# Kernel tuning notes

Measured on AMD Instinct MI355X. Metric: run time of the kernel, lower is better.

Reference implementation:

```python
import jax, jax.numpy as jnp
import numpy as np

N, E, CIN, COUT = 50000, 800000, 61, 64
EPS = 1e-5


def batchnorm(h, g, b):
    # BatchNorm1d in training mode: batch stats (biased variance), affine
    m = jnp.mean(h, axis=0)
    v = jnp.var(h, axis=0)
    return g * (h - m) * jax.lax.rsqrt(v + EPS) + b


def setup_inputs() -> dict:
    key = jax.random.key(0)
    ks = jax.random.split(key, 7)
    x = jax.random.normal(ks[0], (N, CIN), jnp.float32)
    pos = jax.random.normal(ks[1], (N, 3), jnp.float32)
    edge_index = jax.random.randint(ks[2], (2, E), 0, N, dtype=jnp.int64)
    s1 = 1.0 / np.sqrt(CIN + 3)
    s2 = 1.0 / np.sqrt(COUT)
    ss = 1.0 / np.sqrt(CIN)
    W1 = jax.random.normal(ks[3], (CIN + 3, COUT), jnp.float32) * s1
    b1 = jnp.zeros((COUT,), jnp.float32)
    W2 = jax.random.normal(ks[4], (COUT, COUT), jnp.float32) * s2
    b2 = jnp.zeros((COUT,), jnp.float32)
    Ws = jax.random.normal(ks[5], (CIN, COUT), jnp.float32) * ss
    bs = jnp.zeros((COUT,), jnp.float32)
    ones = jnp.ones((COUT,), jnp.float32)
    zeros = jnp.zeros((COUT,), jnp.float32)
    return {
        "x": x, "pos": pos, "edge_index": edge_index,
        "W1": W1, "b1": b1, "g1": ones, "be1": zeros,
        "W2": W2, "b2": b2, "g2": ones, "be2": zeros,
        "Ws": Ws, "bs": bs, "gs": ones, "bes": zeros,
        "gf": ones, "bef": zeros,
    }


def reference(x, pos, edge_index, W1, b1, g1, be1, W2, b2, g2, be2,
              Ws, bs, gs, bes, gf, bef):
    src, dst = edge_index[0], edge_index[1]  # j -> i (source_to_target)
    # per-edge message: [x_j, pos_j - pos_i]  -> [E, CIN+3]
    msg = jnp.concatenate([x[src], pos[src] - pos[dst]], axis=-1)
    # local_nn = MLP([CIN+3, COUT, COUT]) with per-layer Lin -> ReLU -> BN
    h = batchnorm(jax.nn.relu(msg @ W1 + b1), g1, be1)
    h = batchnorm(jax.nn.relu(h @ W2 + b2), g2, be2)
    # scatter-max aggregation to destination nodes
    agg = jax.ops.segment_max(h, dst, num_segments=N)
    agg = jnp.where(jnp.isneginf(agg), 0.0, agg)  # nodes with no incoming edges
    # residual shortcut (Linear + BN since CIN != COUT)
    identity = batchnorm(x @ Ws + bs, gs, bes)
    return jax.nn.relu(batchnorm(agg, gf, bef) + identity)
```

## Files before the change

kernel.cpp:

```cpp
#include <hip/hip_runtime.h>

#define CIN 61
constexpr float EPS = 1e-5f;
constexpr double SCALE = 16777216.0;

using s16x8 = __attribute__((ext_vector_type(8))) short;
using fx4   = __attribute__((ext_vector_type(4))) float;

static __device__ __forceinline__ unsigned short f2bf(float f) {
  unsigned int u = __float_as_uint(f);
  u = (u + 0x7fffu + ((u >> 16) & 1u)) >> 16;
  return (unsigned short)u;
}
static __device__ __forceinline__ float bf2f(unsigned short h) {
  return __uint_as_float(((unsigned int)h) << 16);
}

__device__ __forceinline__ void stat_reduce(float val, float* red, long long* dst_ll) {
  int tid = threadIdx.x;
  red[tid] = val;
  __syncthreads();
  if (tid < 64) {
    float t = red[tid] + red[tid + 64] + red[tid + 128] + red[tid + 192];
    atomicAdd((unsigned long long*)&dst_ll[tid],
              (unsigned long long)(long long)((double)t * SCALE));
  }
  __syncthreads();
}

__global__ __launch_bounds__(256) void k_node(
    const float* __restrict__ x, const float* __restrict__ W1,
    const float* __restrict__ b1, const float* __restrict__ Ws,
    const float* __restrict__ bs, unsigned short* __restrict__ y,
    unsigned short* __restrict__ s_out, long long* __restrict__ stats, int N,
    const int* __restrict__ ei, unsigned int* __restrict__ hist,
    unsigned short* __restrict__ rank, int E) {
  const int tid = threadIdx.x, lane = tid & 63, wv = tid >> 6;
  float w1r[64], wsr[64];
#pragma unroll
  for (int k = 0; k < 64; ++k) {
    w1r[k] = (k < CIN) ? W1[k * 64 + lane] : 0.f;
    wsr[k] = (k < CIN) ? Ws[k * 64 + lane] : 0.f;
  }
  const float b1v = b1[lane], bsv = bs[lane];
  __shared__ float lrow[4][64];
  __shared__ float red[256];
  float ssum = 0.f, ssq = 0.f;
  const int nq = N >> 2;
  for (int q = blockIdx.x; q < nq; q += gridDim.x) {
    const int n = (q << 2) + wv;
    lrow[wv][lane] = (lane < CIN) ? x[(size_t)n * CIN + lane] : 0.f;
    __builtin_amdgcn_wave_barrier();
    float a0 = b1v, a1 = 0.f, a2 = 0.f, a3 = 0.f;
    float c0 = bsv, c1 = 0.f, c2 = 0.f, c3 = 0.f;
    const float4* rr = (const float4*)&lrow[wv][0];
#pragma unroll
    for (int k4 = 0; k4 < 16; ++k4) {
      float4 v = rr[k4];
      a0 = fmaf(v.x, w1r[4 * k4 + 0], a0);
      a1 = fmaf(v.y, w1r[4 * k4 + 1], a1);
      a2 = fmaf(v.z, w1r[4 * k4 + 2], a2);
      a3 = fmaf(v.w, w1r[4 * k4 + 3], a3);
      c0 = fmaf(v.x, wsr[4 * k4 + 0], c0);
      c1 = fmaf(v.y, wsr[4 * k4 + 1], c1);
      c2 = fmaf(v.z, wsr[4 * k4 + 2], c2);
      c3 = fmaf(v.w, wsr[4 * k4 + 3], c3);
    }
    y[(size_t)n * 64 + lane] = f2bf((a0 + a1) + (a2 + a3));
    const float sacc = (c0 + c1) + (c2 + c3);
    s_out[(size_t)n * 64 + lane] = f2bf(sacc);
    ssum += sacc;
    ssq = fmaf(sacc, sacc, ssq);
    __builtin_amdgcn_wave_barrier();
  }
  stat_reduce(ssum, red, stats + 256);
  stat_reduce(ssq, red, stats + 320);
  for (int i = blockIdx.x * 256 + tid; i < E; i += gridDim.x * 256) {
    const int dst = ei[E + i];
    rank[i] = (unsigned short)atomicAdd(&hist[dst], 1u);
  }
}

__global__ __launch_bounds__(256) void k_scan1(
    const unsigned int* __restrict__ hist, unsigned int* __restrict__ bsum) {
  const int tid = threadIdx.x, lane = tid & 63, wv = tid >> 6;
  const uint4 v = ((const uint4*)(hist + blockIdx.x * 1024))[tid];
  unsigned int s = v.x + v.y + v.z + v.w;
#pragma unroll
  for (int off = 1; off < 64; off <<= 1) s += __shfl_xor(s, off);
  __shared__ unsigned int wsum[4];
  if (lane == 0) wsum[wv] = s;
  __syncthreads();
  if (tid == 0) bsum[blockIdx.x] = wsum[0] + wsum[1] + wsum[2] + wsum[3];
}

__global__ __launch_bounds__(256) void k_scan3(
    const unsigned int* __restrict__ hist, const unsigned int* __restrict__ bsum,
    unsigned int* __restrict__ cursor0) {
  const int tid = threadIdx.x, lane = tid & 63, wv = tid >> 6;
  __shared__ unsigned int s_boff;
  if (tid < 64) {
    unsigned int v = (tid < blockIdx.x) ? bsum[tid] : 0u;
#pragma unroll
    for (int off = 1; off < 64; off <<= 1) v += __shfl_xor(v, off);
    if (tid == 0) s_boff = v;
  }
  const uint4 v = ((const uint4*)(hist + blockIdx.x * 1024))[tid];
  const unsigned int s = v.x + v.y + v.z + v.w;
  unsigned int incl = s;
#pragma unroll
  for (int off = 1; off < 64; off <<= 1) {
    unsigned int u = __shfl_up(incl, off);
    if (lane >= off) incl += u;
  }
  __shared__ unsigned int wtot[4];
  if (lane == 63) wtot[wv] = incl;
  __syncthreads();
  unsigned int wb = s_boff;
#pragma unroll
  for (int k = 0; k < 4; ++k) wb += (k < wv) ? wtot[k] : 0u;
  const unsigned int ex = wb + incl - s;
  uint4 o;
  o.x = ex; o.y = ex + v.x; o.z = o.y + v.y; o.w = o.z + v.z;
  ((uint4*)(cursor0 + blockIdx.x * 1024))[tid] = o;
}

__global__ __launch_bounds__(256) void k_edge1(
    const int* __restrict__ ei, const float* __restrict__ pos,
    const unsigned short* __restrict__ y, const float* __restrict__ W1,
    const unsigned int* __restrict__ cursor0, const unsigned short* __restrict__ rank,
    unsigned short* __restrict__ t1S, long long* __restrict__ stats, int E) {
  const int tid = threadIdx.x, lane = tid & 63, wv = tid >> 6;
  const int g8 = lane >> 3, c8 = lane & 7;
  float wp[3][8];
#pragma unroll
  for (int d = 0; d < 3; ++d)
#pragma unroll
    for (int i = 0; i < 8; ++i) wp[d][i] = W1[(61 + d) * 64 + 8 * c8 + i];
  float ssum[8] = {0.f, 0.f, 0.f, 0.f, 0.f, 0.f, 0.f, 0.f};
  float ssq[8]  = {0.f, 0.f, 0.f, 0.f, 0.f, 0.f, 0.f, 0.f};
  const int ngrp = E >> 3;
  const int nw = gridDim.x * 4;
  for (int q = blockIdx.x * 4 + wv; q < ngrp; q += 4 * nw) {
    const int qB = q + nw, qC = q + 2 * nw, qD = q + 3 * nw;
    const bool hB = qB < ngrp, hC = qC < ngrp, hD = qD < ngrp;
    const int eA = (q << 3) + g8;
    const int eB = hB ? (qB << 3) + g8 : eA;
    const int eC = hC ? (qC << 3) + g8 : eA;
    const int eD = hD ? (qD << 3) + g8 : eA;
    const int srcA = ei[eA], dstA = ei[E + eA];
    const int srcB = ei[eB], dstB = ei[E + eB];
    const int srcC = ei[eC], dstC = ei[E + eC];
    const int srcD = ei[eD], dstD = ei[E + eD];
    float pvA = 0.f, pvB = 0.f, pvC = 0.f, pvD = 0.f;
    if (c8 < 3) {
      pvA = pos[srcA * 3 + c8] - pos[dstA * 3 + c8];
      pvB = pos[srcB * 3 + c8] - pos[dstB * 3 + c8];
      pvC = pos[srcC * 3 + c8] - pos[dstC * 3 + c8];
      pvD = pos[srcD * 3 + c8] - pos[dstD * 3 + c8];
    }
    const s16x8 yA = *(const s16x8*)(y + (unsigned)srcA * 64u + 8u * (unsigned)c8);
    const s16x8 yB = *(const s16x8*)(y + (unsigned)srcB * 64u + 8u * (unsigned)c8);
    const s16x8 yC = *(const s16x8*)(y + (unsigned)srcC * 64u + 8u * (unsigned)c8);
    const s16x8 yD = *(const s16x8*)(y + (unsigned)srcD * 64u + 8u * (unsigned)c8);
    unsigned offA = 0, offB = 0, offC = 0, offD = 0;
    if (c8 == 0) {
      offA = cursor0[dstA] + rank[eA];
      offB = cursor0[dstB] + rank[eB];
      offC = cursor0[dstC] + rank[eC];
      offD = cursor0[dstD] + rank[eD];
    }
#define EDGE1_BODY(PV, YV, OFFV)                                                \
    {                                                                           \
      const float p0 = __shfl(PV, g8 * 8 + 0);                                  \
      const float p1 = __shfl(PV, g8 * 8 + 1);                                  \
      const float p2 = __shfl(PV, g8 * 8 + 2);                                  \
      const unsigned off = __shfl(OFFV, g8 * 8 + 0);                            \
      union { s16x8 v; unsigned short s[8]; } tb;                               \
      _Pragma("unroll")                                                         \
      for (int i = 0; i < 8; ++i) {                                             \
        float v = bf2f((unsigned short)YV[i]);                                  \
        v = fmaf(p0, wp[0][i], v);                                              \
        v = fmaf(p1, wp[1][i], v);                                              \
        v = fmaf(p2, wp[2][i], v);                                              \
        v = fmaxf(v, 0.f);                                                      \
        ssum[i] += v;                                                           \
        ssq[i] = fmaf(v, v, ssq[i]);                                            \
        tb.s[i] = f2bf(v);                                                      \
      }                                                                         \
      *(s16x8*)(t1S + (size_t)off * 64 + 8 * c8) = tb.v;                        \
    }
    EDGE1_BODY(pvA, yA, offA)
    if (hB) EDGE1_BODY(pvB, yB, offB)
    if (hC) EDGE1_BODY(pvC, yC, offC)
    if (hD) EDGE1_BODY(pvD, yD, offD)
#undef EDGE1_BODY
  }
#pragma unroll
  for (int i = 0; i < 8; ++i) {
    ssum[i] += __shfl_xor(ssum[i], 8);
    ssum[i] += __shfl_xor(ssum[i], 16);
    ssum[i] += __shfl_xor(ssum[i], 32);
    ssq[i] += __shfl_xor(ssq[i], 8);
    ssq[i] += __shfl_xor(ssq[i], 16);
    ssq[i] += __shfl_xor(ssq[i], 32);
  }
  __shared__ float sred[2][64];
  if (tid < 128) ((float*)sred)[tid] = 0.f;
  __syncthreads();
  if (g8 == 0) {
#pragma unroll
    for (int i = 0; i < 8; ++i) {
      atomicAdd(&sred[0][8 * c8 + i], ssum[i]);
      atomicAdd(&sred[1][8 * c8 + i], ssq[i]);
    }
  }
  __syncthreads();
  if (tid < 64) {
    atomicAdd((unsigned long long*)&stats[0 + tid],
              (unsigned long long)(long long)((double)sred[0][tid] * SCALE));
    atomicAdd((unsigned long long*)&stats[64 + tid],
              (unsigned long long)(long long)((double)sred[1][tid] * SCALE));
  }
}

__global__ void k_coefA(const long long* __restrict__ stats,
                        const float* __restrict__ g1, const float* __restrict__ be1,
                        const float* __restrict__ W2, const float* __restrict__ b2,
                        unsigned short* __restrict__ bFpack,
                        float* __restrict__ biasF, double invE) {
  const int c = threadIdx.x;
  __shared__ float a1s[64], c1s[64], b2sh[64];
  double m = (double)stats[c] * invE;
  double v = (double)stats[64 + c] * invE - m * m;
  float a = g1[c] * rsqrtf((float)v + EPS);
  a1s[c] = a;
  c1s[c] = fmaf(-(float)m, a, be1[c]);
  __syncthreads();
  float acc = b2[c];
  for (int k = 0; k < 64; ++k) acc = fmaf(c1s[k], W2[k * 64 + c], acc);
  b2sh[c] = acc;
  const int lg = c >> 4, l15 = c & 15;
#pragma unroll
  for (int t = 0; t < 4; ++t)
#pragma unroll
    for (int s = 0; s < 2; ++s)
#pragma unroll
      for (int i = 0; i < 8; ++i) {
        const int k = s * 32 + lg * 8 + i;
        bFpack[c * 64 + t * 16 + s * 8 + i] = f2bf(a1s[k] * W2[k * 64 + l15 + 16 * t]);
      }
  __syncthreads();
  float4 bf;
  bf.x = b2sh[l15]; bf.y = b2sh[l15 + 16]; bf.z = b2sh[l15 + 32]; bf.w = b2sh[l15 + 48];
  ((float4*)biasF)[c] = bf;
}

__global__ __launch_bounds__(256) void k_edge2(
    const unsigned short* __restrict__ t1S, const unsigned int* __restrict__ cursor0,
    const unsigned short* __restrict__ bFpack, const float* __restrict__ biasF,
    long long* __restrict__ stats, float* __restrict__ agg, int N) {
  const int tid = threadIdx.x, lane = tid & 63, wv = tid >> 6;
  const int l15 = lane & 15, lg = lane >> 4;
  s16x8 bF[4][2];
  {
    const s16x8* bfp = (const s16x8*)(bFpack + (size_t)lane * 64);
#pragma unroll
    for (int t = 0; t < 4; ++t)
#pragma unroll
      for (int s = 0; s < 2; ++s) bF[t][s] = bfp[t * 2 + s];
  }
  float bias[4];
  {
    const float4 bv = ((const float4*)biasF)[lane];
    bias[0] = bv.x; bias[1] = bv.y; bias[2] = bv.z; bias[3] = bv.w;
  }
  float ssum[4] = {0.f, 0.f, 0.f, 0.f}, ssq[4] = {0.f, 0.f, 0.f, 0.f};
  const int nw = gridDim.x * 4;
  for (int d = blockIdx.x * 4 + wv; d < N; d += nw) {
    const unsigned lo = cursor0[d];
    const unsigned deg = cursor0[d + 1] - lo;
    if (deg == 0) continue;
    const unsigned last = lo + deg - 1u;
    float mx[4] = {0.f, 0.f, 0.f, 0.f};
    for (unsigned base = 0; base < deg; base += 16u) {
      unsigned gr = lo + base + (unsigned)l15;
      if (gr > last) gr = last;
      const unsigned short* ar = t1S + (size_t)gr * 64 + (unsigned)(lg * 8);
      const s16x8 aF0 = *(const s16x8*)ar;
      const s16x8 aF1 = *(const s16x8*)(ar + 32);
      fx4 acc[4];
#pragma unroll
      for (int t = 0; t < 4; ++t) {
        acc[t][0] = bias[t]; acc[t][1] = bias[t];
        acc[t][2] = bias[t]; acc[t][3] = bias[t];
      }
#pragma unroll
      for (int t = 0; t < 4; ++t) {
        acc[t] = __builtin_amdgcn_mfma_f32_16x16x32_bf16(aF0, bF[t][0], acc[t], 0, 0, 0);
        acc[t] = __builtin_amdgcn_mfma_f32_16x16x32_bf16(aF1, bF[t][1], acc[t], 0, 0, 0);
      }
      const int rem = (int)(deg - base);
#pragma unroll
      for (int t = 0; t < 4; ++t)
#pragma unroll
        for (int j = 0; j < 4; ++j) {
          const float v = fmaxf(acc[t][j], 0.f);
          mx[t] = fmaxf(mx[t], v);
          const int row = lg * 4 + j;
          if (row < rem) {
            ssum[t] += v;
            ssq[t] = fmaf(v, v, ssq[t]);
          }
        }
    }
#pragma unroll
    for (int t = 0; t < 4; ++t) {
      mx[t] = fmaxf(mx[t], __shfl_xor(mx[t], 16));
      mx[t] = fmaxf(mx[t], __shfl_xor(mx[t], 32));
    }
    const float val = (lg == 0) ? mx[0] : (lg == 1) ? mx[1] : (lg == 2) ? mx[2] : mx[3];
    agg[(size_t)d * 64 + (unsigned)(l15 + 16 * lg)] = val;
  }
#pragma unroll
  for (int t = 0; t < 4; ++t) {
    ssum[t] += __shfl_xor(ssum[t], 16); ssum[t] += __shfl_xor(ssum[t], 32);
    ssq[t]  += __shfl_xor(ssq[t], 16);  ssq[t]  += __shfl_xor(ssq[t], 32);
  }
  __shared__ float sred[2][64];
  if (tid < 128) ((float*)sred)[tid] = 0.f;
  __syncthreads();
  if (lg == 0) {
#pragma unroll
    for (int t = 0; t < 4; ++t) {
      atomicAdd(&sred[0][l15 + 16 * t], ssum[t]);
      atomicAdd(&sred[1][l15 + 16 * t], ssq[t]);
    }
  }
  __syncthreads();
  if (tid < 64) {
    atomicAdd((unsigned long long*)&stats[128 + tid],
              (unsigned long long)(long long)((double)sred[0][tid] * SCALE));
    atomicAdd((unsigned long long*)&stats[192 + tid],
              (unsigned long long)(long long)((double)sred[1][tid] * SCALE));
  }
}

__global__ __launch_bounds__(256) void k_aggfix(
    const float* __restrict__ agg, const unsigned int* __restrict__ hist,
    long long* __restrict__ stats, int total) {
  const int tid = threadIdx.x;
  __shared__ float red[256];
  float ssum = 0.f, ssq = 0.f, kcf = 0.f;
  const int step = gridDim.x * 256;
  for (int i = blockIdx.x * 256 + tid; i < total; i += step) {
    if (hist[i >> 6]) {
      const float v = agg[i];
      ssum += v;
      ssq = fmaf(v, v, ssq);
      if ((i & 63) == 0) kcf += 1.f;
    }
  }
  stat_reduce(ssum, red, stats + 384);
  stat_reduce(ssq, red, stats + 448);
  stat_reduce(kcf, red, stats + 512);
}

__global__ void k_coefB(const long long* __restrict__ stats,
                        const float* __restrict__ g2, const float* __restrict__ be2,
                        const float* __restrict__ gs, const float* __restrict__ bes,
                        const float* __restrict__ gf, const float* __restrict__ bef,
                        float* __restrict__ coef, double invE, double invN, int N) {
  const int c = threadIdx.x;
  double m2 = (double)stats[128 + c] * invE;
  double v2 = (double)stats[192 + c] * invE - m2 * m2;
  float a2 = g2[c] * rsqrtf((float)v2 + EPS);
  float c2 = fmaf(-(float)m2, a2, be2[c]);
  double mS = (double)stats[256 + c] * invN;
  double vS = (double)stats[320 + c] * invN - mS * mS;
  float aS = gs[c] * rsqrtf((float)vS + EPS);
  float cS = fmaf(-(float)mS, aS, bes[c]);
  double su = (double)stats[384 + c] / SCALE;
  double qu = (double)stats[448 + c] / SCALE;
  double K  = (double)stats[512] / SCALE;
  double sv = (double)a2 * su + (double)c2 * K;
  double qv = (double)a2 * a2 * qu + 2.0 * a2 * c2 * su + (double)c2 * c2 * K;
  double mv = sv / N;
  double vv = qv / N - mv * mv;
  float aF = gf[c] * rsqrtf((float)vv + EPS);
  float cF = fmaf(-(float)mv, aF, bef[c]);
  coef[c]       = aF * a2;
  coef[64 + c]  = fmaf(aF, c2, cF);
  coef[128 + c] = cF;
  coef[192 + c] = aS;
  coef[256 + c] = cS;
}

__global__ __launch_bounds__(256) void k_final(
    const float* __restrict__ agg, const unsigned int* __restrict__ hist,
    const unsigned short* __restrict__ sbuf, const float* __restrict__ coef,
    float* __restrict__ out, int total) {
  int i = blockIdx.x * 256 + threadIdx.x;
  if (i >= total) return;
  const int c = i & 63;
  float base;
  if (hist[i >> 6])
    base = fmaf(coef[c], agg[i], coef[64 + c]);
  else
    base = coef[128 + c];
  const float sv = fmaf(coef[192 + c], bf2f(sbuf[i]), coef[256 + c]);
  out[i] = fmaxf(base + sv, 0.f);
}

extern "C" void kernel_launch(void* const* d_in, const int* in_sizes, int n_in,
                              void* d_out, int out_size, void* d_ws, size_t ws_size,
                              hipStream_t stream) {
  const float* x   = (const float*)d_in[0];
  const float* pos = (const float*)d_in[1];
  const int*   ei  = (const int*)d_in[2];
  const float* W1  = (const float*)d_in[3];
  const float* b1  = (const float*)d_in[4];
  const float* g1  = (const float*)d_in[5];
  const float* be1 = (const float*)d_in[6];
  const float* W2  = (const float*)d_in[7];
  const float* b2  = (const float*)d_in[8];
  const float* g2  = (const float*)d_in[9];
  const float* be2 = (const float*)d_in[10];
  const float* Ws  = (const float*)d_in[11];
  const float* bs  = (const float*)d_in[12];
  const float* gs  = (const float*)d_in[13];
  const float* bes = (const float*)d_in[14];
  const float* gf  = (const float*)d_in[15];
  const float* bef = (const float*)d_in[16];
  const int N = in_sizes[0] / CIN;
  const int E = in_sizes[2] / 2;

  char* ws = (char*)d_ws;
  const size_t o_stats = 0;
  const size_t o_bsum  = 4608;
  const size_t o_hist  = 8192;
  const size_t zeroEnd = o_hist + 200704;
  const size_t o_agg   = zeroEnd;
  const size_t o_curs0 = o_agg + (size_t)N * 256;
  const size_t o_coef  = o_curs0 + 200704;
  const size_t o_frag  = o_coef + 4096;
  const size_t o_rank  = o_frag + 12288;
  const size_t o_ybuf  = o_rank + (size_t)E * 2;
  const size_t o_sbuf  = o_ybuf + (size_t)N * 128;
  const size_t o_t1S   = o_sbuf + (size_t)N * 128;

  long long* stats      = (long long*)(ws + o_stats);
  unsigned int* bsum    = (unsigned int*)(ws + o_bsum);
  unsigned int* hist    = (unsigned int*)(ws + o_hist);
  float* agg            = (float*)(ws + o_agg);
  unsigned int* cursor0 = (unsigned int*)(ws + o_curs0);
  float* coef           = (float*)(ws + o_coef);
  unsigned short* bFpack= (unsigned short*)(ws + o_frag);
  float* biasF          = (float*)(ws + o_frag + 8192);
  unsigned short* rank  = (unsigned short*)(ws + o_rank);
  unsigned short* ybuf  = (unsigned short*)(ws + o_ybuf);
  unsigned short* sbuf  = (unsigned short*)(ws + o_sbuf);
  unsigned short* t1S   = (unsigned short*)(ws + o_t1S);

  const double invE = 1.0 / (SCALE * (double)E);
  const double invN = 1.0 / (SCALE * (double)N);
  const int total = N * 64;
  const int nScanBlk = 49;

  hipMemsetAsync(d_ws, 0, zeroEnd, stream);

  hipLaunchKernelGGL(k_node, dim3(1024), dim3(256), 0, stream,
                     x, W1, b1, Ws, bs, ybuf, sbuf, stats, N, ei, hist, rank, E);
  hipLaunchKernelGGL(k_scan1, dim3(nScanBlk), dim3(256), 0, stream, hist, bsum);
  hipLaunchKernelGGL(k_scan3, dim3(nScanBlk), dim3(256), 0, stream,
                     hist, bsum, cursor0);
  hipLaunchKernelGGL(k_edge1, dim3(2048), dim3(256), 0, stream,
                     ei, pos, ybuf, W1, cursor0, rank, t1S, stats, E);
  hipLaunchKernelGGL(k_coefA, dim3(1), dim3(64), 0, stream,
                     stats, g1, be1, W2, b2, bFpack, biasF, invE);
  hipLaunchKernelGGL(k_edge2, dim3(2048), dim3(256), 0, stream,
                     t1S, cursor0, bFpack, biasF, stats, agg, N);
  hipLaunchKernelGGL(k_aggfix, dim3(1024), dim3(256), 0, stream,
                     agg, hist, stats, total);
  hipLaunchKernelGGL(k_coefB, dim3(1), dim3(64), 0, stream,
                     stats, g2, be2, gs, bes, gf, bef, coef, invE, invN, N);
  hipLaunchKernelGGL(k_final, dim3((total + 255) / 256), dim3(256), 0, stream,
                     agg, hist, sbuf, coef, (float*)d_out, total);
}
```

Measured before the change: 252.0 us.

## Fuse agg statistics into edge2 and split node kernel by weight matrix

Per-node max sums, sums of squares and non-empty node counts are now accumulated inside the edge2 kernel, so the separate aggfix pass that re-read the whole agg buffer is removed. The node kernel now splits its blocks into two groups: one computes the W1 projection, the other computes the shortcut projection plus its stats and the destination histogram. This halves the weight registers each thread holds, which should raise occupancy. It also shifts the histogram work onto the shortcut group only, which could unbalance the two groups.

```diff
diff --git a/kernel.cpp b/kernel.cpp
--- a/kernel.cpp
+++ b/kernel.cpp
@@ -34,50 +34,66 @@
     const float* __restrict__ bs, unsigned short* __restrict__ y,
     unsigned short* __restrict__ s_out, long long* __restrict__ stats, int N,
     const int* __restrict__ ei, unsigned int* __restrict__ hist,
-    unsigned short* __restrict__ rank, int E) {
+    unsigned short* __restrict__ rank, int E, int G) {
   const int tid = threadIdx.x, lane = tid & 63, wv = tid >> 6;
-  float w1r[64], wsr[64];
-#pragma unroll
-  for (int k = 0; k < 64; ++k) {
-    w1r[k] = (k < CIN) ? W1[k * 64 + lane] : 0.f;
-    wsr[k] = (k < CIN) ? Ws[k * 64 + lane] : 0.f;
-  }
-  const float b1v = b1[lane], bsv = bs[lane];
   __shared__ float lrow[4][64];
   __shared__ float red[256];
-  float ssum = 0.f, ssq = 0.f;
   const int nq = N >> 2;
-  for (int q = blockIdx.x; q < nq; q += gridDim.x) {
-    const int n = (q << 2) + wv;
-    lrow[wv][lane] = (lane < CIN) ? x[(size_t)n * CIN + lane] : 0.f;
-    __builtin_amdgcn_wave_barrier();
-    float a0 = b1v, a1 = 0.f, a2 = 0.f, a3 = 0.f;
-    float c0 = bsv, c1 = 0.f, c2 = 0.f, c3 = 0.f;
-    const float4* rr = (const float4*)&lrow[wv][0];
-#pragma unroll
-    for (int k4 = 0; k4 < 16; ++k4) {
-      float4 v = rr[k4];
-      a0 = fmaf(v.x, w1r[4 * k4 + 0], a0);
-      a1 = fmaf(v.y, w1r[4 * k4 + 1], a1);
-      a2 = fmaf(v.z, w1r[4 * k4 + 2], a2);
-      a3 = fmaf(v.w, w1r[4 * k4 + 3], a3);
-      c0 = fmaf(v.x, wsr[4 * k4 + 0], c0);
-      c1 = fmaf(v.y, wsr[4 * k4 + 1], c1);
-      c2 = fmaf(v.z, wsr[4 * k4 + 2], c2);
-      c3 = fmaf(v.w, wsr[4 * k4 + 3], c3);
-    }
-    y[(size_t)n * 64 + lane] = f2bf((a0 + a1) + (a2 + a3));
-    const float sacc = (c0 + c1) + (c2 + c3);
-    s_out[(size_t)n * 64 + lane] = f2bf(sacc);
-    ssum += sacc;
-    ssq = fmaf(sacc, sacc, ssq);
-    __builtin_amdgcn_wave_barrier();
-  }
-  stat_reduce(ssum, red, stats + 256);
-  stat_reduce(ssq, red, stats + 320);
-  for (int i = blockIdx.x * 256 + tid; i < E; i += gridDim.x * 256) {
-    const int dst = ei[E + i];
-    rank[i] = (unsigned short)atomicAdd(&hist[dst], 1u);
+  if ((int)blockIdx.x < G) {
+    float w[64];
+#pragma unroll
+    for (int k = 0; k < 64; ++k) w[k] = (k < CIN) ? W1[k * 64 + lane] : 0.f;
+    const float bv = b1[lane];
+    for (int q = blockIdx.x; q < nq; q += G) {
+      const int n = (q << 2) + wv;
+      lrow[wv][lane] = (lane < CIN) ? x[(size_t)n * CIN + lane] : 0.f;
+      __builtin_amdgcn_wave_barrier();
+      float a0 = bv, a1 = 0.f, a2 = 0.f, a3 = 0.f;
+      const float4* rr = (const float4*)&lrow[wv][0];
+#pragma unroll
+      for (int k4 = 0; k4 < 16; ++k4) {
+        float4 v = rr[k4];
+        a0 = fmaf(v.x, w[4 * k4 + 0], a0);
+        a1 = fmaf(v.y, w[4 * k4 + 1], a1);
+        a2 = fmaf(v.z, w[4 * k4 + 2], a2);
+        a3 = fmaf(v.w, w[4 * k4 + 3], a3);
+      }
+      y[(size_t)n * 64 + lane] = f2bf((a0 + a1) + (a2 + a3));
+      __builtin_amdgcn_wave_barrier();
+    }
+  } else {
+    const int b = blockIdx.x - G, nB = gridDim.x - G;
+    float w[64];
+#pragma unroll
+    for (int k = 0; k < 64; ++k) w[k] = (k < CIN) ? Ws[k * 64 + lane] : 0.f;
+    const float bv = bs[lane];
+    float ssum = 0.f, ssq = 0.f;
+    for (int q = b; q < nq; q += nB) {
+      const int n = (q << 2) + wv;
+      lrow[wv][lane] = (lane < CIN) ? x[(size_t)n * CIN + lane] : 0.f;
+      __builtin_amdgcn_wave_barrier();
+      float a0 = bv, a1 = 0.f, a2 = 0.f, a3 = 0.f;
+      const float4* rr = (const float4*)&lrow[wv][0];
+#pragma unroll
+      for (int k4 = 0; k4 < 16; ++k4) {
+        float4 v = rr[k4];
+        a0 = fmaf(v.x, w[4 * k4 + 0], a0);
+        a1 = fmaf(v.y, w[4 * k4 + 1], a1);
+        a2 = fmaf(v.z, w[4 * k4 + 2], a2);
+        a3 = fmaf(v.w, w[4 * k4 + 3], a3);
+      }
+      const float sacc = (a0 + a1) + (a2 + a3);
+      s_out[(size_t)n * 64 + lane] = f2bf(sacc);
+      ssum += sacc;
+      ssq = fmaf(sacc, sacc, ssq);
+      __builtin_amdgcn_wave_barrier();
+    }
+    stat_reduce(ssum, red, stats + 256);
+    stat_reduce(ssq, red, stats + 320);
+    for (int i = b * 256 + tid; i < E; i += nB * 256) {
+      const int dst = ei[E + i];
+      rank[i] = (unsigned short)atomicAdd(&hist[dst], 1u);
+    }
   }
 }
 
@@ -276,11 +292,14 @@
     bias[0] = bv.x; bias[1] = bv.y; bias[2] = bv.z; bias[3] = bv.w;
   }
   float ssum[4] = {0.f, 0.f, 0.f, 0.f}, ssq[4] = {0.f, 0.f, 0.f, 0.f};
+  float msum[4] = {0.f, 0.f, 0.f, 0.f}, msq[4] = {0.f, 0.f, 0.f, 0.f};
+  float kc = 0.f;
   const int nw = gridDim.x * 4;
   for (int d = blockIdx.x * 4 + wv; d < N; d += nw) {
     const unsigned lo = cursor0[d];
     const unsigned deg = cursor0[d + 1] - lo;
     if (deg == 0) continue;
+    kc += 1.f;
     const unsigned last = lo + deg - 1u;
     float mx[4] = {0.f, 0.f, 0.f, 0.f};
     for (unsigned base = 0; base < deg; base += 16u) {
@@ -319,6 +338,13 @@
       mx[t] = fmaxf(mx[t], __shfl_xor(mx[t], 16));
       mx[t] = fmaxf(mx[t], __shfl_xor(mx[t], 32));
     }
+    if (lg == 0) {
+#pragma unroll
+      for (int t = 0; t < 4; ++t) {
+        msum[t] += mx[t];
+        msq[t] = fmaf(mx[t], mx[t], msq[t]);
+      }
+    }
     const float val = (lg == 0) ? mx[0] : (lg == 1) ? mx[1] : (lg == 2) ? mx[2] : mx[3];
     agg[(size_t)d * 64 + (unsigned)(l15 + 16 * lg)] = val;
   }
@@ -327,43 +353,35 @@
     ssum[t] += __shfl_xor(ssum[t], 16); ssum[t] += __shfl_xor(ssum[t], 32);
     ssq[t]  += __shfl_xor(ssq[t], 16);  ssq[t]  += __shfl_xor(ssq[t], 32);
   }
-  __shared__ float sred[2][64];
-  if (tid < 128) ((float*)sred)[tid] = 0.f;
+  __shared__ float sred[4][64];
+  __shared__ float kcs;
+  if (tid < 256) ((float*)sred)[tid] = 0.f;
+  if (tid == 0) kcs = 0.f;
   __syncthreads();
   if (lg == 0) {
 #pragma unroll
     for (int t = 0; t < 4; ++t) {
       atomicAdd(&sred[0][l15 + 16 * t], ssum[t]);
       atomicAdd(&sred[1][l15 + 16 * t], ssq[t]);
-    }
-  }
+      atomicAdd(&sred[2][l15 + 16 * t], msum[t]);
+      atomicAdd(&sred[3][l15 + 16 * t], msq[t]);
+    }
+  }
+  if (lane == 0) atomicAdd(&kcs, kc);
   __syncthreads();
   if (tid < 64) {
     atomicAdd((unsigned long long*)&stats[128 + tid],
               (unsigned long long)(long long)((double)sred[0][tid] * SCALE));
     atomicAdd((unsigned long long*)&stats[192 + tid],
               (unsigned long long)(long long)((double)sred[1][tid] * SCALE));
-  }
-}
-
-__global__ __launch_bounds__(256) void k_aggfix(
-    const float* __restrict__ agg, const unsigned int* __restrict__ hist,
-    long long* __restrict__ stats, int total) {
-  const int tid = threadIdx.x;
-  __shared__ float red[256];
-  float ssum = 0.f, ssq = 0.f, kcf = 0.f;
-  const int step = gridDim.x * 256;
-  for (int i = blockIdx.x * 256 + tid; i < total; i += step) {
-    if (hist[i >> 6]) {
-      const float v = agg[i];
-      ssum += v;
-      ssq = fmaf(v, v, ssq);
-      if ((i & 63) == 0) kcf += 1.f;
-    }
-  }
-  stat_reduce(ssum, red, stats + 384);
-  stat_reduce(ssq, red, stats + 448);
-  stat_reduce(kcf, red, stats + 512);
+    atomicAdd((unsigned long long*)&stats[384 + tid],
+              (unsigned long long)(long long)((double)sred[2][tid] * SCALE));
+    atomicAdd((unsigned long long*)&stats[448 + tid],
+              (unsigned long long)(long long)((double)sred[3][tid] * SCALE));
+  }
+  if (tid == 0)
+    atomicAdd((unsigned long long*)&stats[512],
+              (unsigned long long)(long long)((double)kcs * SCALE));
 }
 
 __global__ void k_coefB(const long long* __restrict__ stats,
@@ -470,7 +488,7 @@
   hipMemsetAsync(d_ws, 0, zeroEnd, stream);
 
   hipLaunchKernelGGL(k_node, dim3(1024), dim3(256), 0, stream,
-                     x, W1, b1, Ws, bs, ybuf, sbuf, stats, N, ei, hist, rank, E);
+                     x, W1, b1, Ws, bs, ybuf, sbuf, stats, N, ei, hist, rank, E, 448);
   hipLaunchKernelGGL(k_scan1, dim3(nScanBlk), dim3(256), 0, stream, hist, bsum);
   hipLaunchKernelGGL(k_scan3, dim3(nScanBlk), dim3(256), 0, stream,
                      hist, bsum, cursor0);
@@ -480,8 +498,6 @@
                      stats, g1, be1, W2, b2, bFpack, biasF, invE);
   hipLaunchKernelGGL(k_edge2, dim3(2048), dim3(256), 0, stream,
                      t1S, cursor0, bFpack, biasF, stats, agg, N);
-  hipLaunchKernelGGL(k_aggfix, dim3(1024), dim3(256), 0, stream,
-                     agg, hist, stats, total);
   hipLaunchKernelGGL(k_coefB, dim3(1), dim3(64), 0, stream,
                      stats, g2, be2, gs, bes, gf, bef, coef, invE, invN, N);
   hipLaunchKernelGGL(k_final, dim3((total + 255) / 256), dim3(256), 0, stream,
```

Result: faster. 227.2 us (median of 2 runs) (-9.9%).
